# Optimization experiments

Hardware: AMD Instinct MI355X
Metric: run time of the kernel (lower is better)

## Reference

```python
import jax, jax.numpy as jnp
import numpy as np

T, B, DIM, N = 2048, 16, 1024, 64


def setup_inputs() -> dict:
    key = jax.random.key(0)
    ks = jax.random.split(key, 6)
    # xavier-uniform-ish scale for [N, DIM] linear weights
    lim = float(np.sqrt(6.0 / (DIM + N)))
    mk = lambda k: jax.random.uniform(k, (N, DIM), jnp.float32, -lim, lim)
    return {
        "x": jax.random.normal(ks[0], (T, B, DIM), jnp.float32),
        "S": jnp.zeros((B, N, N), jnp.float32),
        "W_k": mk(ks[1]),
        "W_v": mk(ks[2]),
        "W_q": mk(ks[3]),
        "W_alpha": mk(ks[4]),
        "d_alpha": jnp.full((N,), 0.1, jnp.float32),
        "b_alpha": jnp.full((N,), 2.0, jnp.float32),
    }


def reference(x, S, W_k, W_v, W_q, W_alpha, d_alpha, b_alpha):
    # Projections for the whole sequence at once: [T, B, N]
    k_all = jnp.einsum('tbd,nd->tbn', x, W_k)
    v_all = jnp.einsum('tbd,nd->tbn', x, W_v)
    q_all = jnp.einsum('tbd,nd->tbn', x, W_q)
    a_all = jnp.einsum('tbd,nd->tbn', x, W_alpha)

    def step(S, inp):
        k, v, q, ax = inp  # each [B, N]
        retrieved = jnp.einsum('bij,bj->bi', S, k)                 # [B, N]
        alpha = jax.nn.sigmoid(ax + d_alpha * retrieved + b_alpha)  # [B, N]
        outer_vk = v[:, :, None] * k[:, None, :]                    # [B, N, N]
        S = alpha[:, :, None] * S + (1.0 - alpha[:, :, None]) * outer_vk
        out = jnp.einsum('bij,bj->bi', S, q)                        # [B, N]
        out = out * jax.nn.silu(out)
        return S, out

    S_final, output = jax.lax.scan(step, S, (k_all, v_all, q_all, a_all))
    return output, S_final
```

## Files before the change

### kernel.cpp

```cpp
#include <hip/hip_runtime.h>
#include <hip/hip_bf16.h>

#define T_STEPS 2048
#define BATCH 16
#define DIM 1024
#define NDIM 64
#define M_TOTAL (T_STEPS * BATCH)
#define STRIDE (BATCH * NDIM)
#define CH 32

typedef __attribute__((ext_vector_type(8))) short bf16x8;
typedef __attribute__((ext_vector_type(4))) float f32x4;
typedef __attribute__((ext_vector_type(2))) float f32x2;

#define NEG_LOG2E -1.44269504088896f

__device__ inline unsigned pk_bf(float lo, float hi) {
    __hip_bfloat162 h = __float22bfloat162_rn(float2{lo, hi});
    return *(unsigned*)&h;
}

template <int CTRL>
__device__ inline float dpp_add(float x) {
    int v = __builtin_amdgcn_update_dpp(0, __float_as_int(x), CTRL, 0xF, 0xF, true);
    return x + __int_as_float(v);
}
__device__ inline float red16(float x) {
    x = dpp_add<0xB1>(x);
    x = dpp_add<0x4E>(x);
    x = dpp_add<0x141>(x);
    x = dpp_add<0x140>(x);
    return x;
}
__device__ inline float fast_sigmoid(float z) {
    return __builtin_amdgcn_rcpf(1.f + __expf(-z));
}

#define AS1 __attribute__((address_space(1)))
#define AS3 __attribute__((address_space(3)))
__device__ inline void gl_lds16(const float* g, float* l) {
    __builtin_amdgcn_global_load_lds((const AS1 unsigned*)g, (AS3 unsigned*)l, 16, 0, 0);
}
__device__ inline void gl_lds16s(const unsigned short* g, unsigned short* l) {
    __builtin_amdgcn_global_load_lds((const AS1 unsigned*)g, (AS3 unsigned*)l, 16, 0, 0);
}
__device__ inline void gl_lds4(const float* g, float* l) {
    __builtin_amdgcn_global_load_lds((const AS1 unsigned*)g, (AS3 unsigned*)l, 4, 0, 0);
}
#define WAIT_VM0 do { __builtin_amdgcn_s_waitcnt(0x0F70); asm volatile("" ::: "memory"); } while (0)

__global__ __launch_bounds__(256) void pack_w(
    const float* __restrict__ Wk, const float* __restrict__ Wq,
    const float* __restrict__ Wv, const float* __restrict__ Wa,
    unsigned short* __restrict__ Wb) {
    int n = blockIdx.x;
    int sel = n >> 6;
    const float* W = (sel == 0) ? Wk : (sel == 1) ? Wq : (sel == 2) ? Wv : Wa;
    int k4 = threadIdx.x * 4;
    float4 f = *(const float4*)(W + (size_t)(n & 63) * DIM + k4);
    uint2 u;
    u.x = pk_bf(f.x, f.y);
    u.y = pk_bf(f.z, f.w);
    *(uint2*)(Wb + (size_t)n * DIM + k4) = u;
}

__global__ __launch_bounds__(256, 2) void proj_kernel(
    const float* __restrict__ x, const unsigned short* __restrict__ Wb,
    const float* __restrict__ ba, float* __restrict__ Kp, float* __restrict__ Qp,
    float* __restrict__ VAi) {
    __shared__ float sA[128 * 64];
    __shared__ unsigned short sB[128 * 64];

    const int m0 = blockIdx.x * 128;
    const int ntile = blockIdx.y;
    const int tid = threadIdx.x;
    const int wv = tid >> 6, lane = tid & 63, lrow = lane & 15, quad = lane >> 4;
    const int wm = wv & 1, wn = wv >> 1;

    f32x4 acc[4][4];
#pragma unroll
    for (int a = 0; a < 4; a++)
#pragma unroll
        for (int b = 0; b < 4; b++) acc[a][b] = (f32x4)(0.f);

    const float* xg = x + (size_t)(m0 + (tid >> 4)) * DIM + (tid & 15) * 4;
    const unsigned short* wg = Wb + (size_t)(ntile * 128 + (tid >> 3)) * DIM + (tid & 7) * 8;

    for (int it = 0; it < 16; ++it) {
        const int k0 = it * 64;
        __syncthreads();
#pragma unroll
        for (int j = 0; j < 8; ++j)
            gl_lds16(xg + (size_t)(16 * j) * DIM + k0, &sA[(tid + 256 * j) * 4]);
#pragma unroll
        for (int j = 0; j < 4; ++j)
            gl_lds16s(wg + (size_t)(32 * j) * DIM + k0, &sB[(tid + 256 * j) * 8]);
        WAIT_VM0;
        __syncthreads();

#pragma unroll
        for (int ks = 0; ks < 2; ++ks) {
            bf16x8 af[4];
#pragma unroll
            for (int mt = 0; mt < 4; ++mt) {
                const float* pa = &sA[(wm * 64 + mt * 16 + lrow) * 64 + ks * 32 + quad * 8];
                float4 lo = ((const float4*)pa)[0], hi = ((const float4*)pa)[1];
                unsigned pk[4] = {pk_bf(lo.x, lo.y), pk_bf(lo.z, lo.w),
                                  pk_bf(hi.x, hi.y), pk_bf(hi.z, hi.w)};
                af[mt] = *(bf16x8*)pk;
            }
#pragma unroll
            for (int nt = 0; nt < 4; ++nt) {
                bf16x8 bfr = *(const bf16x8*)&sB[(wn * 64 + nt * 16 + lrow) * 64 + ks * 32 + quad * 8];
#pragma unroll
                for (int mt = 0; mt < 4; ++mt)
                    acc[mt][nt] = __builtin_amdgcn_mfma_f32_16x16x32_bf16(af[mt], bfr, acc[mt][nt], 0, 0, 0);
            }
        }
    }

    const int g2 = ntile * 2 + wn;
    float bav[4];
    if (g2 == 3) {
#pragma unroll
        for (int nt = 0; nt < 4; ++nt) bav[nt] = ba[nt * 16 + lrow];
    }
#pragma unroll
    for (int mt = 0; mt < 4; ++mt)
#pragma unroll
        for (int nt = 0; nt < 4; ++nt) {
            int col = nt * 16 + lrow;
#pragma unroll
            for (int reg = 0; reg < 4; ++reg) {
                int m = m0 + wm * 64 + mt * 16 + quad * 4 + reg;
                float vvv = acc[mt][nt][reg];
                if (g2 == 0) Kp[(size_t)m * 64 + col] = vvv;
                else if (g2 == 1) Qp[(size_t)m * 64 + col] = vvv;
                else if (g2 == 2) VAi[(size_t)m * 128 + col * 2] = vvv;
                else VAi[(size_t)m * 128 + col * 2 + 1] = NEG_LOG2E * (vvv + bav[nt]);
            }
        }
}

__global__ __launch_bounds__(256) void kq_kernel(
    const float* __restrict__ Kp, const float* __restrict__ Qp,
    float* __restrict__ kq, float* __restrict__ kk) {
    int m = blockIdx.x * 16 + (threadIdx.x >> 4);
    int c = threadIdx.x & 15;
    float4 k = *(const float4*)(Kp + (size_t)m * 64 + c * 4);
    float4 q = *(const float4*)(Qp + (size_t)m * 64 + c * 4);
    float4 kn = {0.f, 0.f, 0.f, 0.f};
    if (m + BATCH < M_TOTAL) kn = *(const float4*)(Kp + (size_t)(m + BATCH) * 64 + c * 4);
    float pq = k.x * q.x + k.y * q.y + k.z * q.z + k.w * q.w;
    float pk = k.x * kn.x + k.y * kn.y + k.z * kn.z + k.w * kn.w;
    pq = red16(pq);
    pk = red16(pk);
    if (c == 0) { kq[m] = pq; kk[m] = pk; }
}

__global__ __launch_bounds__(64, 1) void recur_kernel(
    const float* __restrict__ Kp, const float* __restrict__ Qp,
    const float* __restrict__ VAi, const float* __restrict__ KQp,
    const float* __restrict__ KKp,
    const float* __restrict__ S0, const float* __restrict__ d_alpha,
    float* __restrict__ out, float* __restrict__ Sout) {
    __shared__ float Kl[2][CH][64];
    __shared__ float Ql[2][CH][64];
    __shared__ float VAl[2][CH][8];
    __shared__ float KQl[2][64];
    __shared__ float KKl[2][64];
    __shared__ float Ol[CH][4];

    int b = blockIdx.y, g = blockIdx.x, lane = threadIdx.x;
    int r = lane >> 4, c = lane & 15, i = g * 4 + r, c4 = c * 4;

    float4 sv = *(const float4*)(S0 + ((size_t)b * NDIM + i) * NDIM + c4);
    f32x2 s01 = {sv.x, sv.y}, s23 = {sv.z, sv.w};
    float da2 = d_alpha[i] * NEG_LOG2E;

    const float* Kbase = Kp + (size_t)b * NDIM + (size_t)(lane >> 4) * STRIDE + (lane & 15) * 4;
    const float* Qbase = Qp + (size_t)b * NDIM + (size_t)(lane >> 4) * STRIDE + (lane & 15) * 4;
    const float* VAbase = VAi + (size_t)b * 128 + g * 8 + (lane & 1) * 4 + (size_t)(lane >> 1) * 2048;
    const float* KQbase = KQp + b + (size_t)(lane & 31) * BATCH;
    const float* KKbase = KKp + b + (size_t)(lane & 31) * BATCH;
    const float* Kgl = Kp + (size_t)b * NDIM + c4;

    auto load_chunk = [&](int t0, int buf) {
#pragma unroll
        for (int j = 0; j < 8; ++j) {
            gl_lds16(Kbase + (size_t)(t0 + j * 4) * STRIDE, &Kl[buf][j * 4][0]);
            gl_lds16(Qbase + (size_t)(t0 + j * 4) * STRIDE, &Ql[buf][j * 4][0]);
        }
        gl_lds16(VAbase + (size_t)t0 * 2048, &VAl[buf][0][0]);
        gl_lds4(KQbase + (size_t)t0 * BATCH, &KQl[buf][0]);
        gl_lds4(KKbase + (size_t)t0 * BATCH, &KKl[buf][0]);
    };

    load_chunk(0, 0);
    WAIT_VM0;

    f32x2 kc01, kc23, kn01[2], kn23[2], q01[2], q23[2], va[2];
    float kqv[2], kkv[2], rk;
    {
        const float* Kb0 = &Kl[0][0][0];
        const float* Qb0 = &Ql[0][0][0];
        f32x4 k0 = *(const f32x4*)(Kb0 + c4);
        kc01 = k0.lo; kc23 = k0.hi;
#pragma unroll
        for (int u = 0; u < 2; ++u) {
            f32x4 kk_ = *(const f32x4*)(Kb0 + (u + 1) * 64 + c4);
            kn01[u] = kk_.lo; kn23[u] = kk_.hi;
            f32x4 qq = *(const f32x4*)(Qb0 + u * 64 + c4);
            q01[u] = qq.lo; q23[u] = qq.hi;
            va[u] = *(const f32x2*)&VAl[0][u][r * 2];
            kqv[u] = KQl[0][u];
            kkv[u] = KKl[0][u];
        }
        f32x2 p = kc01 * s01;
        p = kc23 * s23 + p;
        rk = red16(p.x + p.y);
    }

    for (int j = 0; j < T_STEPS / CH; ++j) {
        int cb = j & 1;
        if (j + 1 < T_STEPS / CH) load_chunk((j + 1) * CH, cb ^ 1);
        f32x4 kb = *(const f32x4*)(Kgl + (size_t)((j + 1) * CH) * STRIDE);

        const float* Kb = &Kl[cb][0][0];
        const float* Qb = &Ql[cb][0][0];
        const float* Vb = &VAl[cb][0][0];
        const float* Qk = &KQl[cb][0];
        const float* Kk = &KKl[cb][0];

#pragma unroll
        for (int tl = 0; tl < CH; ++tl) {
            int sl = tl & 1;
            f32x2 knA = kn01[sl], knB = kn23[sl];
            f32x2 q0v = q01[sl], q1v = q23[sl];
            f32x2 vva = va[sl];
            float kqs = kqv[sl], kks = kkv[sl];
            if (tl < CH - 2) {
                f32x4 qq = *(const f32x4*)(Qb + (tl + 2) * 64 + c4);
                q01[sl] = qq.lo; q23[sl] = qq.hi;
                va[sl] = *(const f32x2*)&Vb[(tl + 2) * 8 + r * 2];
                kqv[sl] = Qk[tl + 2];
                kkv[sl] = Kk[tl + 2];
            }
            if (tl < CH - 3) {
                f32x4 kk_ = *(const f32x4*)(Kb + (tl + 3) * 64 + c4);
                kn01[sl] = kk_.lo; kn23[sl] = kk_.hi;
            } else if (tl == CH - 3) {
                kn01[sl] = kb.lo; kn23[sl] = kb.hi;
            }

            f32x2 pq_ = q0v * s01; pq_ = q1v * s23 + pq_;
            f32x2 pk_ = knA * s01; pk_ = knB * s23 + pk_;
            float rq = red16(pq_.x + pq_.y);
            float ck = red16(pk_.x + pk_.y);

            float v = vva.x;
            f32x2 w01 = v * kc01, w23 = v * kc23;
            f32x2 d01 = s01 - w01, d23 = s23 - w23;
            float vkk = v * kks, vkq = v * kqs;
            float ckm = ck - vkk, rqm = rq - vkq;

            float alpha = __builtin_amdgcn_rcpf(1.f + __builtin_amdgcn_exp2f(fmaf(da2, rk, vva.y)));
            rk = fmaf(alpha, ckm, vkk);

            f32x2 a2 = {alpha, alpha};
            s01 = w01 + a2 * d01;
            s23 = w23 + a2 * d23;

            float o = fmaf(alpha, rqm, vkq);
            float ov = o * o * fast_sigmoid(o);
            if (c == 0) Ol[tl][r] = ov;
            kc01 = knA; kc23 = knB;
        }
        WAIT_VM0;

        if (lane < 32) {
            float4 t4 = *(const float4*)&Ol[lane][0];
            *(float4*)(out + ((size_t)(j * CH + lane) * BATCH + b) * NDIM + g * 4) = t4;
        }

        if (j + 1 < T_STEPS / CH) {
            int nb = cb ^ 1;
            const float* Kn = &Kl[nb][0][0];
            const float* Qn = &Ql[nb][0][0];
#pragma unroll
            for (int u = 0; u < 2; ++u) {
                f32x4 kk_ = *(const f32x4*)(Kn + (u + 1) * 64 + c4);
                kn01[u] = kk_.lo; kn23[u] = kk_.hi;
                f32x4 qq = *(const f32x4*)(Qn + u * 64 + c4);
                q01[u] = qq.lo; q23[u] = qq.hi;
                va[u] = *(const f32x2*)&VAl[nb][u][r * 2];
                kqv[u] = KQl[nb][u];
                kkv[u] = KKl[nb][u];
            }
        }
    }

    float* so = Sout + ((size_t)b * NDIM + i) * NDIM + c4;
    *(float4*)so = float4{s01.x, s01.y, s23.x, s23.y};
}

extern "C" void kernel_launch(void* const* d_in, const int* in_sizes, int n_in,
                              void* d_out, int out_size, void* d_ws, size_t ws_size,
                              hipStream_t stream) {
    const float* x  = (const float*)d_in[0];
    const float* S0 = (const float*)d_in[1];
    const float* Wk = (const float*)d_in[2];
    const float* Wv = (const float*)d_in[3];
    const float* Wq = (const float*)d_in[4];
    const float* Wa = (const float*)d_in[5];
    const float* da = (const float*)d_in[6];
    const float* ba = (const float*)d_in[7];

    float* out = (float*)d_out;
    float* Sout = out + (size_t)T_STEPS * BATCH * NDIM;

    const size_t per = (size_t)M_TOTAL * NDIM;
    float* Kp  = (float*)d_ws;
    float* Qp  = Kp + per;
    float* VAi = Qp + per;
    float* kq  = VAi + 2 * per;
    float* kk  = kq + M_TOTAL;
    unsigned short* Wb = (unsigned short*)(kk + M_TOTAL);

    pack_w<<<dim3(256), dim3(256), 0, stream>>>(Wk, Wq, Wv, Wa, Wb);
    proj_kernel<<<dim3(M_TOTAL / 128, 2), dim3(256), 0, stream>>>(x, Wb, ba, Kp, Qp, VAi);
    kq_kernel<<<dim3(M_TOTAL / 16), dim3(256), 0, stream>>>(Kp, Qp, kq, kk);
    recur_kernel<<<dim3(16, BATCH), dim3(64), 0, stream>>>(Kp, Qp, VAi, kq, kk, S0, da, out, Sout);
}
```

Baseline: 501.6 us.

## Software-pipeline recurrence step: prefetch across chunk boundary and defer output sigmoid

Restructures the per-step recurrence loop so the exp2 for the next alpha is issued early, and the q/k reductions for the next step are paired into interleaved DPP reductions. The output silu is deferred by one step to take it off the critical dependency chain. LDS prefetches now wrap into the next chunk buffer, which removes the per-chunk reload block and the global K load. The wait for the next chunk moves to step 28 so the prefetch window crosses chunks, at the cost of more complex indexing and higher register use.

```diff
diff --git a/kernel.cpp b/kernel.cpp
--- a/kernel.cpp
+++ b/kernel.cpp
@@ -32,8 +32,16 @@
     x = dpp_add<0x140>(x);
     return x;
 }
-__device__ inline float fast_sigmoid(float z) {
-    return __builtin_amdgcn_rcpf(1.f + __expf(-z));
+__device__ inline void red16x2(float& a, float& b) {
+    a = dpp_add<0xB1>(a);  b = dpp_add<0xB1>(b);
+    a = dpp_add<0x4E>(a);  b = dpp_add<0x4E>(b);
+    a = dpp_add<0x141>(a); b = dpp_add<0x141>(b);
+    a = dpp_add<0x140>(a); b = dpp_add<0x140>(b);
+}
+__device__ inline float dot4(f32x4 a, f32x4 b) {
+    f32x2 t = a.lo * b.lo;
+    t = a.hi * b.hi + t;
+    return t.x + t.y;
 }
 
 #define AS1 __attribute__((address_space(1)))
@@ -174,8 +182,7 @@
     int b = blockIdx.y, g = blockIdx.x, lane = threadIdx.x;
     int r = lane >> 4, c = lane & 15, i = g * 4 + r, c4 = c * 4;
 
-    float4 sv = *(const float4*)(S0 + ((size_t)b * NDIM + i) * NDIM + c4);
-    f32x2 s01 = {sv.x, sv.y}, s23 = {sv.z, sv.w};
+    f32x4 sv = *(const f32x4*)(S0 + ((size_t)b * NDIM + i) * NDIM + c4);
     float da2 = d_alpha[i] * NEG_LOG2E;
 
     const float* Kbase = Kp + (size_t)b * NDIM + (size_t)(lane >> 4) * STRIDE + (lane & 15) * 4;
@@ -183,7 +190,6 @@
     const float* VAbase = VAi + (size_t)b * 128 + g * 8 + (lane & 1) * 4 + (size_t)(lane >> 1) * 2048;
     const float* KQbase = KQp + b + (size_t)(lane & 31) * BATCH;
     const float* KKbase = KKp + b + (size_t)(lane & 31) * BATCH;
-    const float* Kgl = Kp + (size_t)b * NDIM + c4;
 
     auto load_chunk = [&](int t0, int buf) {
 #pragma unroll
@@ -199,109 +205,121 @@
     load_chunk(0, 0);
     WAIT_VM0;
 
-    f32x2 kc01, kc23, kn01[2], kn23[2], q01[2], q23[2], va[2];
-    float kqv[2], kkv[2], rk;
+    f32x4 kreg[4], qreg[2];
+    f32x2 va2[2];
+    float kq2[2], kk2[2];
+    float ee, ckm, rqm, vkq, vkk, v_cur, o_prev = 0.f;
+
     {
-        const float* Kb0 = &Kl[0][0][0];
-        const float* Qb0 = &Ql[0][0][0];
-        f32x4 k0 = *(const f32x4*)(Kb0 + c4);
-        kc01 = k0.lo; kc23 = k0.hi;
-#pragma unroll
-        for (int u = 0; u < 2; ++u) {
-            f32x4 kk_ = *(const f32x4*)(Kb0 + (u + 1) * 64 + c4);
-            kn01[u] = kk_.lo; kn23[u] = kk_.hi;
-            f32x4 qq = *(const f32x4*)(Qb0 + u * 64 + c4);
-            q01[u] = qq.lo; q23[u] = qq.hi;
-            va[u] = *(const f32x2*)&VAl[0][u][r * 2];
-            kqv[u] = KQl[0][u];
-            kkv[u] = KKl[0][u];
-        }
-        f32x2 p = kc01 * s01;
-        p = kc23 * s23 + p;
-        rk = red16(p.x + p.y);
+        const float* K0 = &Kl[0][0][0];
+        const float* Q0 = &Ql[0][0][0];
+        kreg[0] = *(const f32x4*)(K0 + 0 * 64 + c4);
+        kreg[1] = *(const f32x4*)(K0 + 1 * 64 + c4);
+        kreg[2] = *(const f32x4*)(K0 + 2 * 64 + c4);
+        kreg[3] = *(const f32x4*)(K0 + 3 * 64 + c4);
+        qreg[1] = *(const f32x4*)(Q0 + 1 * 64 + c4);
+        va2[1] = *(const f32x2*)&VAl[0][1][r * 2];
+        kq2[1] = KQl[0][1];
+        kk2[1] = KKl[0][1];
+        f32x4 q0 = *(const f32x4*)(Q0 + 0 * 64 + c4);
+        f32x2 va0 = *(const f32x2*)&VAl[0][0][r * 2];
+        float kq0 = KQl[0][0], kk0 = KKl[0][0];
+
+        float rk0 = dot4(kreg[0], sv);
+        float rq0 = dot4(q0, sv);
+        float ck0 = dot4(kreg[1], sv);
+        red16x2(rk0, rq0);
+        ck0 = red16(ck0);
+
+        ee = __builtin_amdgcn_exp2f(fmaf(da2, rk0, va0.y));
+        vkq = va0.x * kq0;
+        vkk = va0.x * kk0;
+        rqm = rq0 - vkq;
+        ckm = ck0 - vkk;
+        v_cur = va0.x;
     }
 
+#define STEP(tl) do {                                                          \
+    const int cs_ = ((tl) + 1) & 1, ls_ = (tl) & 1;                            \
+    f32x4 qv_ = qreg[cs_];                                                     \
+    f32x2 vax_ = va2[cs_];                                                     \
+    float kq1_ = kq2[cs_], kk1_ = kk2[cs_];                                    \
+    f32x4 kv_ = kreg[(tl) & 3];                                                \
+    f32x4 kmv_ = kreg[((tl) + 2) & 3];                                         \
+    {   const int i2_ = (tl) + 2;                                              \
+        const float* Qs_ = (i2_ < CH) ? Qc : Qn;                               \
+        const float* Vs_ = (i2_ < CH) ? Vc : Vn;                               \
+        const float* QKs_ = (i2_ < CH) ? QKc : QKn;                            \
+        const float* KKs_ = (i2_ < CH) ? KKc : KKn;                            \
+        const int m2_ = i2_ & (CH - 1);                                        \
+        qreg[ls_] = *(const f32x4*)(Qs_ + m2_ * 64 + c4);                      \
+        va2[ls_] = *(const f32x2*)(Vs_ + m2_ * 8 + r * 2);                     \
+        kq2[ls_] = QKs_[m2_];                                                  \
+        kk2[ls_] = KKs_[m2_];                                                  \
+        const int i4_ = (tl) + 4;                                              \
+        const float* Ks_ = (i4_ < CH) ? Kc : Kn_;                              \
+        kreg[(tl) & 3] = *(const f32x4*)(Ks_ + (i4_ & (CH - 1)) * 64 + c4); }  \
+    float alpha_ = __builtin_amdgcn_rcpf(1.f + ee);                            \
+    f32x4 w_ = v_cur * kv_;                                                    \
+    f32x4 dd_ = sv - w_;                                                       \
+    float rk1_ = fmaf(alpha_, ckm, vkk);                                       \
+    sv = w_ + alpha_ * dd_;                                                    \
+    float z_ = fmaf(da2, rk1_, vax_.y);                                        \
+    float o_ = fmaf(alpha_, rqm, vkq);                                         \
+    ee = __builtin_amdgcn_exp2f(z_);                                           \
+    f32x2 tq_ = qv_.lo * sv.lo;  tq_ = qv_.hi * sv.hi + tq_;                   \
+    f32x2 tk_ = kmv_.lo * sv.lo; tk_ = kmv_.hi * sv.hi + tk_;                  \
+    float pq_ = tq_.x + tq_.y, pk_ = tk_.x + tk_.y;                            \
+    red16x2(pq_, pk_);                                                         \
+    float vkqn_ = vax_.x * kq1_, vkkn_ = vax_.x * kk1_;                        \
+    rqm = pq_ - vkqn_;                                                         \
+    ckm = pk_ - vkkn_;                                                         \
+    vkq = vkqn_; vkk = vkkn_;                                                  \
+    if ((tl) > 0) {                                                            \
+        float eo_ = __builtin_amdgcn_exp2f(o_prev * NEG_LOG2E);                \
+        float so_ = __builtin_amdgcn_rcpf(1.f + eo_);                          \
+        float ov_ = o_prev * o_prev * so_;                                     \
+        if (c == 0) Ol[(tl) - 1][r] = ov_; }                                   \
+    o_prev = o_;                                                               \
+    v_cur = vax_.x;                                                            \
+} while (0)
+
     for (int j = 0; j < T_STEPS / CH; ++j) {
-        int cb = j & 1;
-        if (j + 1 < T_STEPS / CH) load_chunk((j + 1) * CH, cb ^ 1);
-        f32x4 kb = *(const f32x4*)(Kgl + (size_t)((j + 1) * CH) * STRIDE);
-
-        const float* Kb = &Kl[cb][0][0];
-        const float* Qb = &Ql[cb][0][0];
-        const float* Vb = &VAl[cb][0][0];
-        const float* Qk = &KQl[cb][0];
-        const float* Kk = &KKl[cb][0];
-
-#pragma unroll
-        for (int tl = 0; tl < CH; ++tl) {
-            int sl = tl & 1;
-            f32x2 knA = kn01[sl], knB = kn23[sl];
-            f32x2 q0v = q01[sl], q1v = q23[sl];
-            f32x2 vva = va[sl];
-            float kqs = kqv[sl], kks = kkv[sl];
-            if (tl < CH - 2) {
-                f32x4 qq = *(const f32x4*)(Qb + (tl + 2) * 64 + c4);
-                q01[sl] = qq.lo; q23[sl] = qq.hi;
-                va[sl] = *(const f32x2*)&Vb[(tl + 2) * 8 + r * 2];
-                kqv[sl] = Qk[tl + 2];
-                kkv[sl] = Kk[tl + 2];
-            }
-            if (tl < CH - 3) {
-                f32x4 kk_ = *(const f32x4*)(Kb + (tl + 3) * 64 + c4);
-                kn01[sl] = kk_.lo; kn23[sl] = kk_.hi;
-            } else if (tl == CH - 3) {
-                kn01[sl] = kb.lo; kn23[sl] = kb.hi;
-            }
-
-            f32x2 pq_ = q0v * s01; pq_ = q1v * s23 + pq_;
-            f32x2 pk_ = knA * s01; pk_ = knB * s23 + pk_;
-            float rq = red16(pq_.x + pq_.y);
-            float ck = red16(pk_.x + pk_.y);
-
-            float v = vva.x;
-            f32x2 w01 = v * kc01, w23 = v * kc23;
-            f32x2 d01 = s01 - w01, d23 = s23 - w23;
-            float vkk = v * kks, vkq = v * kqs;
-            float ckm = ck - vkk, rqm = rq - vkq;
-
-            float alpha = __builtin_amdgcn_rcpf(1.f + __builtin_amdgcn_exp2f(fmaf(da2, rk, vva.y)));
-            rk = fmaf(alpha, ckm, vkk);
-
-            f32x2 a2 = {alpha, alpha};
-            s01 = w01 + a2 * d01;
-            s23 = w23 + a2 * d23;
-
-            float o = fmaf(alpha, rqm, vkq);
-            float ov = o * o * fast_sigmoid(o);
-            if (c == 0) Ol[tl][r] = ov;
-            kc01 = knA; kc23 = knB;
-        }
+        const int cb = j & 1, nb = cb ^ 1;
+        if (j + 1 < T_STEPS / CH) load_chunk((j + 1) * CH, nb);
+
+        const float* Kc = &Kl[cb][0][0];
+        const float* Kn_ = &Kl[nb][0][0];
+        const float* Qc = &Ql[cb][0][0];
+        const float* Qn = &Ql[nb][0][0];
+        const float* Vc = &VAl[cb][0][0];
+        const float* Vn = &VAl[nb][0][0];
+        const float* QKc = &KQl[cb][0];
+        const float* QKn = &KQl[nb][0];
+        const float* KKc = &KKl[cb][0];
+        const float* KKn = &KKl[nb][0];
+
+#pragma unroll
+        for (int tl = 0; tl < 28; ++tl) STEP(tl);
         WAIT_VM0;
-
+#pragma unroll
+        for (int tl = 28; tl < 32; ++tl) STEP(tl);
+
+        {
+            float eo = __builtin_amdgcn_exp2f(o_prev * NEG_LOG2E);
+            float so = __builtin_amdgcn_rcpf(1.f + eo);
+            float ov = o_prev * o_prev * so;
+            if (c == 0) Ol[CH - 1][r] = ov;
+        }
         if (lane < 32) {
             float4 t4 = *(const float4*)&Ol[lane][0];
             *(float4*)(out + ((size_t)(j * CH + lane) * BATCH + b) * NDIM + g * 4) = t4;
         }
-
-        if (j + 1 < T_STEPS / CH) {
-            int nb = cb ^ 1;
-            const float* Kn = &Kl[nb][0][0];
-            const float* Qn = &Ql[nb][0][0];
-#pragma unroll
-            for (int u = 0; u < 2; ++u) {
-                f32x4 kk_ = *(const f32x4*)(Kn + (u + 1) * 64 + c4);
-                kn01[u] = kk_.lo; kn23[u] = kk_.hi;
-                f32x4 qq = *(const f32x4*)(Qn + u * 64 + c4);
-                q01[u] = qq.lo; q23[u] = qq.hi;
-                va[u] = *(const f32x2*)&VAl[nb][u][r * 2];
-                kqv[u] = KQl[nb][u];
-                kkv[u] = KKl[nb][u];
-            }
-        }
     }
-
-    float* so = Sout + ((size_t)b * NDIM + i) * NDIM + c4;
-    *(float4*)so = float4{s01.x, s01.y, s23.x, s23.y};
+#undef STEP
+
+    float* so_ = Sout + ((size_t)b * NDIM + i) * NDIM + c4;
+    *(float4*)so_ = float4{sv.x, sv.y, sv.z, sv.w};
 }
 
 extern "C" void kernel_launch(void* const* d_in, const int* in_sizes, int n_in,
```

Measured after the change: 514.0 us. 1.02x slower.
